# Kernel optimization log

Measured on AMD Instinct MI355X. Metric: run time of the kernel, lower is better.

The kernel has to match this reference:

```python
import jax, jax.numpy as jnp
import numpy as np

B, S, D = 4, 2048, 1024
H = 16
HD = D // H  # 64


def setup_inputs() -> dict:
    key = jax.random.key(0)
    ks = jax.random.split(key, 8)
    scale = 1.0 / np.sqrt(D)
    return {
        "hidden_states": jax.random.normal(ks[0], (B, S, D), dtype=jnp.float32),
        "attention_mask": jnp.ones((B, 1, 1, S), dtype=jnp.int32),
        "Wq": jax.random.normal(ks[1], (D, D), dtype=jnp.float32) * scale,
        "bq": jax.random.normal(ks[2], (D,), dtype=jnp.float32) * 0.02,
        "Wk": jax.random.normal(ks[3], (D, D), dtype=jnp.float32) * scale,
        "bk": jax.random.normal(ks[4], (D,), dtype=jnp.float32) * 0.02,
        "Wv": jax.random.normal(ks[5], (D, D), dtype=jnp.float32) * scale,
        "bv": jax.random.normal(ks[6], (D,), dtype=jnp.float32) * 0.02,
    }


def _split_heads(x):
    # [b, t, (h d)] -> [b, h, t, d]
    b, t, _ = x.shape
    return x.reshape(b, t, H, HD).transpose(0, 2, 1, 3)


def reference(hidden_states, attention_mask, Wq, bq, Wk, bk, Wv, bv):
    # Linear projections (torch Linear: x @ W.T + b)
    q = _split_heads(hidden_states @ Wq.T + bq)
    k = _split_heads(hidden_states @ Wk.T + bk)
    v = _split_heads(hidden_states @ Wv.T + bv)

    # scaled dot-product scores: [b, h, s, s]
    scores = jnp.einsum("bhqd,bhkd->bhqk", q, k) / np.sqrt(HD)

    s = scores.shape[-1]
    causal = jnp.tril(jnp.ones((s, s), dtype=bool))[None, None]
    neg_inf = jnp.float32(-jnp.inf)
    scores = jnp.where(causal, scores, neg_inf)
    # attention_mask is 0/1 keep mask: [b, 1, 1, s]
    scores = jnp.where(attention_mask == 0, neg_inf, scores)

    probs = jax.nn.softmax(scores, axis=-1)  # dropout p=0 (eval)
    ctx = jnp.einsum("bhqk,bhkd->bhqd", probs, v)
    # [b, h, t, d] -> [b, t, h*d]
    return ctx.transpose(0, 2, 1, 3).reshape(hidden_states.shape[0], s, D)
```

## Files before the change

kernel.cpp:

```cpp
#include <hip/hip_runtime.h>
#include <hip/hip_bf16.h>
#include <math.h>


#define B_ 4
#define S_ 2048
#define D_ 1024
#define H_ 16
#define HD_ 64
#define M_ (B_ * S_)

typedef unsigned short u16;
typedef unsigned int u32;
typedef __attribute__((ext_vector_type(4))) float f32x4;
typedef __attribute__((ext_vector_type(8))) short bf16x8;

__device__ __forceinline__ u16 f2bfu_rn(float x) {
    u32 u = __builtin_bit_cast(u32, x);
    return (u16)((u + 0x8000u) >> 16);
}

__device__ __forceinline__ void gl2lds16(const void* g, void* l) {
    __builtin_amdgcn_global_load_lds(
        (const __attribute__((address_space(1))) u32*)g,
        (__attribute__((address_space(3))) u32*)l, 16, 0, 0);
}

#define XN  8388608u
#define WN  1048576u
__global__ __launch_bounds__(256) void convert_bf16(
    const float* __restrict__ X,  const float* __restrict__ Wq,
    const float* __restrict__ Wk, const float* __restrict__ Wv,
    u16* __restrict__ Xb, u16* __restrict__ Wqb,
    u16* __restrict__ Wkb, u16* __restrict__ Wvb)
{
    size_t idx = ((size_t)blockIdx.x * 256 + threadIdx.x) * 8;
    const float* src; u16* dst; size_t off;
    if (idx < XN)                { src = X;  dst = Xb;  off = idx; }
    else if (idx < XN + WN)      { src = Wq; dst = Wqb; off = idx - XN; }
    else if (idx < XN + 2 * WN)  { src = Wk; dst = Wkb; off = idx - XN - WN; }
    else                         { src = Wv; dst = Wvb; off = idx - XN - 2 * WN; }
    float4 a = *(const float4*)(src + off);
    float4 b = *(const float4*)(src + off + 4);
    uint4 o;
    o.x = (u32)f2bfu_rn(a.x) | ((u32)f2bfu_rn(a.y) << 16);
    o.y = (u32)f2bfu_rn(a.z) | ((u32)f2bfu_rn(a.w) << 16);
    o.z = (u32)f2bfu_rn(b.x) | ((u32)f2bfu_rn(b.y) << 16);
    o.w = (u32)f2bfu_rn(b.z) | ((u32)f2bfu_rn(b.w) << 16);
    *(uint4*)(dst + off) = o;
}

#define QSCALE 0.18033688011112042f

__global__ __launch_bounds__(512) void qkv_mfma8(
    const u16* __restrict__ Xb,
    const u16* __restrict__ Wqb, const u16* __restrict__ Wkb,
    const u16* __restrict__ Wvb,
    const float* __restrict__ bq, const float* __restrict__ bk,
    const float* __restrict__ bv,
    u16* __restrict__ Qb, u16* __restrict__ Kb, u16* __restrict__ Vtb)
{
    const int which = blockIdx.y;
    const int bxl = ((blockIdx.x & 7) << 5) | (blockIdx.x >> 3);

    const u16* Asrc; const u16* Bsrc; const float* bias; u16* Out;
    int m0, n0;
    if (which == 0)      { Asrc = Xb;  Bsrc = Wqb; bias = bq; Out = Qb;
                           m0 = (bxl >> 2) * 128; n0 = (bxl & 3) * 256; }
    else if (which == 1) { Asrc = Xb;  Bsrc = Wkb; bias = bk; Out = Kb;
                           m0 = (bxl >> 2) * 128; n0 = (bxl & 3) * 256; }
    else                 { Asrc = Wvb; Bsrc = Xb;  bias = bv; Out = Vtb;
                           m0 = (bxl >> 5) * 128; n0 = (bxl & 31) * 256; }

    __shared__ u16 As[3][128][64];
    __shared__ u16 Bs[3][256][64];

    const int t = threadIdx.x;
    const int wave = t >> 6, lane = t & 63;
    const int qd = lane >> 4, l15 = lane & 15;
    const int wm = wave >> 2, wn = wave & 3;

    auto STAGE_A = [&](int tt, int u) {
        const int buf = tt % 3, k0 = tt * 64;
        const int rb = u * 64 + wave * 8;
        const int r  = rb + (lane >> 3);
        const int g  = (lane & 7) ^ (r & 7);
        gl2lds16(Asrc + (size_t)(m0 + r) * D_ + k0 + g * 8, &As[buf][rb][0]);
    };
    auto STAGE_B = [&](int tt, int q) {
        const int buf = tt % 3, k0 = tt * 64;
        const int rb = q * 64 + wave * 8;
        const int r  = rb + (lane >> 3);
        const int g  = (lane & 7) ^ (r & 7);
        gl2lds16(Bsrc + (size_t)(n0 + r) * D_ + k0 + g * 8, &Bs[buf][rb][0]);
    };

    const f32x4 zero = {0.f, 0.f, 0.f, 0.f};
    f32x4 acc[4][4];
#pragma unroll
    for (int i = 0; i < 4; ++i)
#pragma unroll
        for (int j = 0; j < 4; ++j) acc[i][j] = zero;

#pragma unroll
    for (int u = 0; u < 2; ++u) STAGE_A(0, u);
#pragma unroll
    for (int q = 0; q < 4; ++q) STAGE_B(0, q);
#pragma unroll
    for (int u = 0; u < 2; ++u) STAGE_A(1, u);
#pragma unroll
    for (int q = 0; q < 4; ++q) STAGE_B(1, q);
    asm volatile("s_waitcnt vmcnt(6)" ::: "memory");
    __builtin_amdgcn_s_barrier();

    for (int tt = 0; tt < 16; ++tt) {
        const int buf = tt % 3;
        const bool st = tt < 14;
        const int t2 = tt + 2;

        bf16x8 bfv[4][2];
        bf16x8 af[2];

#pragma unroll
        for (int nt = 0; nt < 4; ++nt) {
            const int row = wn * 64 + nt * 16 + l15;
#pragma unroll
            for (int ks = 0; ks < 2; ++ks)
                bfv[nt][ks] = *(const bf16x8*)&Bs[buf][row][((ks * 4 + qd) ^ (row & 7)) * 8];
        }
        {
            const int row = wm * 64 + l15;
#pragma unroll
            for (int ks = 0; ks < 2; ++ks)
                af[ks] = *(const bf16x8*)&As[buf][row][((ks * 4 + qd) ^ (row & 7)) * 8];
        }
        if (st) { STAGE_A(t2, 0); STAGE_A(t2, 1); }
        __builtin_amdgcn_s_barrier();
        asm volatile("s_waitcnt lgkmcnt(0)" ::: "memory");
        __builtin_amdgcn_sched_barrier(0);
        __builtin_amdgcn_s_setprio(1);
#pragma unroll
        for (int ks = 0; ks < 2; ++ks)
#pragma unroll
            for (int nt = 0; nt < 4; ++nt)
                acc[0][nt] = __builtin_amdgcn_mfma_f32_16x16x32_bf16(
                    af[ks], bfv[nt][ks], acc[0][nt], 0, 0, 0);
        __builtin_amdgcn_s_setprio(0);
        __builtin_amdgcn_s_barrier();

#pragma unroll
        for (int mt = 1; mt < 4; ++mt) {
            const int row = wm * 64 + mt * 16 + l15;
#pragma unroll
            for (int ks = 0; ks < 2; ++ks)
                af[ks] = *(const bf16x8*)&As[buf][row][((ks * 4 + qd) ^ (row & 7)) * 8];
            if (st) {
                if (mt == 1)      { STAGE_B(t2, 0); STAGE_B(t2, 1); }
                else if (mt == 2) { STAGE_B(t2, 2); }
                else              { STAGE_B(t2, 3); }
            }
            __builtin_amdgcn_s_barrier();
            asm volatile("s_waitcnt lgkmcnt(0)" ::: "memory");
            __builtin_amdgcn_sched_barrier(0);
            __builtin_amdgcn_s_setprio(1);
#pragma unroll
            for (int ks = 0; ks < 2; ++ks)
#pragma unroll
                for (int nt = 0; nt < 4; ++nt)
                    acc[mt][nt] = __builtin_amdgcn_mfma_f32_16x16x32_bf16(
                        af[ks], bfv[nt][ks], acc[mt][nt], 0, 0, 0);
            __builtin_amdgcn_s_setprio(0);
            if (mt == 3) {
                if (st) asm volatile("s_waitcnt vmcnt(6)" ::: "memory");
                else    asm volatile("s_waitcnt vmcnt(0)" ::: "memory");
            }
            __builtin_amdgcn_s_barrier();
        }
    }

    if (which < 2) {
#pragma unroll
        for (int nt = 0; nt < 4; ++nt) {
            int n = n0 + wn * 64 + nt * 16 + l15;
            float bv_ = bias[n];
            int h = n >> 6, hd = n & 63;
#pragma unroll
            for (int mt = 0; mt < 4; ++mt)
#pragma unroll
                for (int r = 0; r < 4; ++r) {
                    int m = m0 + wm * 64 + mt * 16 + qd * 4 + r;
                    int bb = m >> 11, s = m & 2047;
                    float v = acc[mt][nt][r] + bv_;
                    if (which == 0) v *= QSCALE;
                    Out[(((size_t)(bb * H_ + h)) * S_ + s) * HD_ + hd] = f2bfu_rn(v);
                }
        }
    } else {
#pragma unroll
        for (int mt = 0; mt < 4; ++mt)
#pragma unroll
            for (int r = 0; r < 4; ++r) {
                int f = m0 + wm * 64 + mt * 16 + qd * 4 + r;
                float bv_ = bias[f];
                int h = f >> 6, hd = f & 63;
#pragma unroll
                for (int nt = 0; nt < 4; ++nt) {
                    int tok = n0 + wn * 64 + nt * 16 + l15;
                    int bb = tok >> 11, s = tok & 2047;
                    float v = acc[mt][nt][r] + bv_;
                    Out[(((size_t)(bb * H_ + h)) * HD_ + hd) * S_ + s] = f2bfu_rn(v);
                }
            }
    }
}

__global__ __launch_bounds__(256) void attn_chunk(
    const u16* __restrict__ Qb, const u16* __restrict__ Kb,
    const u16* __restrict__ Vtb, const int* __restrict__ amask,
    float* __restrict__ Oout, float* __restrict__ Opart,
    float* __restrict__ L0, float* __restrict__ L1)
{
    const int bid = blockIdx.x;
    const int x   = bid >> 6;
    const int bh  = ((bid & 7) << 3) | ((bid >> 3) & 7);
    const int b = bh >> 4, h = bh & 15;
    int qt, jt0, jt1; bool second;
    if (x < 32) { qt = 31 - x; jt0 = 0;  jt1 = min(qt, 15); second = false; }
    else        { qt = 63 - x; jt0 = 16; jt1 = qt;          second = true;  }
    const int q0 = qt * 64;

    const int t = threadIdx.x;
    const int wave = t >> 6, lane = t & 63;
    const int qd = lane >> 4, l15 = lane & 15;

    __shared__ u16 Ks[64][64];
    __shared__ u16 Vts[64][64];
    __shared__ u16 Ps[64][72];
    __shared__ float mb[64];

    const size_t base = (size_t)bh * S_ * HD_;
    const u16* Qg = Qb + base;
    const u16* Kg = Kb + base;
    const u16* Vg = Vtb + base;
    const int* am = amask + b * S_;

    bf16x8 qf[2];
    {
        const u16* qrow = Qg + (size_t)(q0 + wave * 16 + l15) * HD_;
        qf[0] = *(const bf16x8*)(qrow + qd * 8);
        qf[1] = *(const bf16x8*)(qrow + 32 + qd * 8);
    }
    bf16x8 onesf;
    {
        short v = (l15 == 0) ? (short)0x3F80 : (short)0;
        onesf = (bf16x8){v, v, v, v, v, v, v, v};
    }

    const f32x4 zero = {0.f, 0.f, 0.f, 0.f};
    f32x4 o[5];
#pragma unroll
    for (int i = 0; i < 5; ++i) o[i] = zero;

    const int qloc = wave * 16 + l15;
    u32* prow32 = (u32*)&Ps[qloc][0];

    for (int jt = jt0; jt <= jt1; ++jt) {
        const int j0 = jt * 64;
        __syncthreads();
#pragma unroll
        for (int i = 0; i < 2; ++i) {
            int r0  = (wave * 2 + i) * 8;
            int row = r0 + (lane >> 3);
            int g   = (lane & 7) ^ (row & 7);
            gl2lds16(Kg + (size_t)(j0 + row) * HD_ + g * 8, &Ks[r0][0]);
            gl2lds16(Vg + (size_t)row * S_ + j0 + g * 8, &Vts[r0][0]);
        }
        if (t < 64) mb[t] = (am[j0 + t] == 0) ? -1e30f : 0.0f;
        __syncthreads();

        f32x4 sacc[4];
#pragma unroll
        for (int nt = 0; nt < 4; ++nt) sacc[nt] = zero;
        __builtin_amdgcn_s_setprio(1);
#pragma unroll
        for (int ks = 0; ks < 2; ++ks) {
#pragma unroll
            for (int nt = 0; nt < 4; ++nt) {
                int arow = nt * 16 + l15;
                int ap = (ks * 4 + qd) ^ (arow & 7);
                bf16x8 kf = *(const bf16x8*)&Ks[arow][ap * 8];
                sacc[nt] = __builtin_amdgcn_mfma_f32_16x16x32_bf16(
                    kf, qf[ks], sacc[nt], 0, 0, 0);
            }
        }
        __builtin_amdgcn_s_setprio(0);

        const bool diag = (jt == qt);
#pragma unroll
        for (int nt = 0; nt < 4; ++nt) {
            float4 m4 = *(const float4*)&mb[nt * 16 + qd * 4];
            float p[4];
#pragma unroll
            for (int r = 0; r < 4; ++r) {
                int kl = nt * 16 + qd * 4 + r;
                float s = sacc[nt][r] + ((const float*)&m4)[r];
                if (diag && kl > qloc) s = -1e30f;
                p[r] = __builtin_amdgcn_exp2f(s);
            }
            uint2 w;
            w.x = (u32)f2bfu_rn(p[0]) | ((u32)f2bfu_rn(p[1]) << 16);
            w.y = (u32)f2bfu_rn(p[2]) | ((u32)f2bfu_rn(p[3]) << 16);
            *(uint2*)&prow32[nt * 8 + qd * 2] = w;
        }

        __builtin_amdgcn_s_setprio(1);
#pragma unroll
        for (int ks = 0; ks < 2; ++ks) {
            int arow = wave * 16 + l15;
            bf16x8 pf = *(const bf16x8*)&Ps[arow][ks * 32 + qd * 8];
#pragma unroll
            for (int nt = 0; nt < 4; ++nt) {
                int brow = nt * 16 + l15;
                int bp = (ks * 4 + qd) ^ (brow & 7);
                bf16x8 vf = *(const bf16x8*)&Vts[brow][bp * 8];
                o[nt] = __builtin_amdgcn_mfma_f32_16x16x32_bf16(
                    pf, vf, o[nt], 0, 0, 0);
            }
            o[4] = __builtin_amdgcn_mfma_f32_16x16x32_bf16(
                pf, onesf, o[4], 0, 0, 0);
        }
        __builtin_amdgcn_s_setprio(0);
    }

    if (!second) {
        if (qt <= 15) {
#pragma unroll
            for (int r = 0; r < 4; ++r) {
                float l = __shfl(o[4][r], lane & 48);
                float inv = 1.0f / l;
                int q = q0 + wave * 16 + qd * 4 + r;
                float* op = Oout + ((size_t)(b * S_ + q)) * D_ + h * HD_;
#pragma unroll
                for (int nt = 0; nt < 4; ++nt)
                    op[nt * 16 + l15] = o[nt][r] * inv;
            }
        } else {
#pragma unroll
            for (int r = 0; r < 4; ++r) {
                int q = q0 + wave * 16 + qd * 4 + r;
                float* op = Oout + ((size_t)(b * S_ + q)) * D_ + h * HD_;
#pragma unroll
                for (int nt = 0; nt < 4; ++nt)
                    op[nt * 16 + l15] = o[nt][r];
                if (l15 == 0) L0[(size_t)bh * S_ + q] = o[4][r];
            }
        }
    } else {
#pragma unroll
        for (int r = 0; r < 4; ++r) {
            int q = q0 + wave * 16 + qd * 4 + r;
            int sh = q - 1024;
            float* op = Opart + ((size_t)bh * 1024 + sh) * HD_;
#pragma unroll
            for (int nt = 0; nt < 4; ++nt)
                op[nt * 16 + l15] = o[nt][r];
            if (l15 == 0) L1[(size_t)bh * 1024 + sh] = o[4][r];
        }
    }
}

__global__ __launch_bounds__(256) void combine(
    float* __restrict__ out, const float* __restrict__ Opart,
    const float* __restrict__ L0, const float* __restrict__ L1)
{
    size_t i = ((size_t)blockIdx.x * 256 + threadIdx.x) * 4;
    int d  = (int)(i & (D_ - 1));
    int bs = (int)(i >> 10);
    int b  = bs >> 10, sh = bs & 1023;
    int s  = sh + 1024;
    int h  = d >> 6;
    int bh = b * H_ + h;
    float l = L0[(size_t)bh * S_ + s] + L1[(size_t)bh * 1024 + sh];
    float inv = 1.0f / l;
    float* op = out + ((size_t)(b * S_ + s)) * D_ + d;
    const float* pp = Opart + ((size_t)bh * 1024 + sh) * HD_ + (d & 63);
    float4 v = *(float4*)op;
    float4 p = *(const float4*)pp;
    v.x = (v.x + p.x) * inv; v.y = (v.y + p.y) * inv;
    v.z = (v.z + p.z) * inv; v.w = (v.w + p.w) * inv;
    *(float4*)op = v;
}

extern "C" void kernel_launch(void* const* d_in, const int* in_sizes, int n_in,
                              void* d_out, int out_size, void* d_ws, size_t ws_size,
                              hipStream_t stream) {
    (void)in_sizes; (void)n_in; (void)out_size; (void)ws_size;
    const float* X    = (const float*)d_in[0];
    const int*   mask = (const int*)d_in[1];
    const float* Wq   = (const float*)d_in[2];
    const float* bq   = (const float*)d_in[3];
    const float* Wk   = (const float*)d_in[4];
    const float* bk   = (const float*)d_in[5];
    const float* Wv   = (const float*)d_in[6];
    const float* bv   = (const float*)d_in[7];
    float* out = (float*)d_out;

    u16* Xb  = (u16*)d_ws;
    u16* Wqb = Xb  + XN;
    u16* Wkb = Wqb + WN;
    u16* Wvb = Wkb + WN;
    u16* Qb  = Wvb + WN;
    u16* Kb  = Qb  + XN;
    u16* Vtb = Kb  + XN;
    float* Opart = (float*)(Vtb + XN);
    float* L0 = Opart + (size_t)64 * 1024 * 64;
    float* L1 = L0 + (size_t)64 * 2048;

    convert_bf16<<<(XN + 3 * WN) / (256 * 8), 256, 0, stream>>>(
        X, Wq, Wk, Wv, Xb, Wqb, Wkb, Wvb);
    qkv_mfma8<<<dim3(256, 3), 512, 0, stream>>>(
        Xb, Wqb, Wkb, Wvb, bq, bk, bv, Qb, Kb, Vtb);
    attn_chunk<<<dim3(3072), 256, 0, stream>>>(
        Qb, Kb, Vtb, mask, out, Opart, L0, L1);
    combine<<<(B_ * 1024 * D_ / 4) / 256, 256, 0, stream>>>(out, Opart, L0, L1);
}
```

Baseline: 243.8 us.

## Enlarge QKV GEMM tile to 256x256 with double-buffered LDS staging

```diff
diff --git a/kernel.cpp b/kernel.cpp
--- a/kernel.cpp
+++ b/kernel.cpp
@@ -61,19 +61,19 @@
     u16* __restrict__ Qb, u16* __restrict__ Kb, u16* __restrict__ Vtb)
 {
     const int which = blockIdx.y;
-    const int bxl = ((blockIdx.x & 7) << 5) | (blockIdx.x >> 3);
+    const int bxl = ((blockIdx.x & 7) << 4) | (blockIdx.x >> 3);
 
     const u16* Asrc; const u16* Bsrc; const float* bias; u16* Out;
     int m0, n0;
     if (which == 0)      { Asrc = Xb;  Bsrc = Wqb; bias = bq; Out = Qb;
-                           m0 = (bxl >> 2) * 128; n0 = (bxl & 3) * 256; }
+                           m0 = (bxl >> 2) * 256; n0 = (bxl & 3) * 256; }
     else if (which == 1) { Asrc = Xb;  Bsrc = Wkb; bias = bk; Out = Kb;
-                           m0 = (bxl >> 2) * 128; n0 = (bxl & 3) * 256; }
+                           m0 = (bxl >> 2) * 256; n0 = (bxl & 3) * 256; }
     else                 { Asrc = Wvb; Bsrc = Xb;  bias = bv; Out = Vtb;
-                           m0 = (bxl >> 5) * 128; n0 = (bxl & 31) * 256; }
-
-    __shared__ u16 As[3][128][64];
-    __shared__ u16 Bs[3][256][64];
+                           m0 = (bxl & 3) * 256; n0 = (bxl >> 2) * 256; }
+
+    __shared__ u16 As[2][256][64];
+    __shared__ u16 Bs[2][256][64];
 
     const int t = threadIdx.x;
     const int wave = t >> 6, lane = t & 63;
@@ -81,46 +81,47 @@
     const int wm = wave >> 2, wn = wave & 3;
 
     auto STAGE_A = [&](int tt, int u) {
-        const int buf = tt % 3, k0 = tt * 64;
+        const int buf = tt & 1, k0 = tt * 64;
         const int rb = u * 64 + wave * 8;
         const int r  = rb + (lane >> 3);
         const int g  = (lane & 7) ^ (r & 7);
         gl2lds16(Asrc + (size_t)(m0 + r) * D_ + k0 + g * 8, &As[buf][rb][0]);
     };
-    auto STAGE_B = [&](int tt, int q) {
-        const int buf = tt % 3, k0 = tt * 64;
-        const int rb = q * 64 + wave * 8;
+    auto STAGE_B = [&](int tt, int u) {
+        const int buf = tt & 1, k0 = tt * 64;
+        const int rb = u * 64 + wave * 8;
         const int r  = rb + (lane >> 3);
         const int g  = (lane & 7) ^ (r & 7);
         gl2lds16(Bsrc + (size_t)(n0 + r) * D_ + k0 + g * 8, &Bs[buf][rb][0]);
     };
 
     const f32x4 zero = {0.f, 0.f, 0.f, 0.f};
-    f32x4 acc[4][4];
-#pragma unroll
-    for (int i = 0; i < 4; ++i)
+    f32x4 acc[8][4];
+#pragma unroll
+    for (int i = 0; i < 8; ++i)
 #pragma unroll
         for (int j = 0; j < 4; ++j) acc[i][j] = zero;
 
 #pragma unroll
-    for (int u = 0; u < 2; ++u) STAGE_A(0, u);
-#pragma unroll
-    for (int q = 0; q < 4; ++q) STAGE_B(0, q);
-#pragma unroll
-    for (int u = 0; u < 2; ++u) STAGE_A(1, u);
-#pragma unroll
-    for (int q = 0; q < 4; ++q) STAGE_B(1, q);
-    asm volatile("s_waitcnt vmcnt(6)" ::: "memory");
+    for (int u = 0; u < 4; ++u) STAGE_A(0, u);
+#pragma unroll
+    for (int u = 0; u < 4; ++u) STAGE_B(0, u);
+    asm volatile("s_waitcnt vmcnt(0)" ::: "memory");
     __builtin_amdgcn_s_barrier();
 
     for (int tt = 0; tt < 16; ++tt) {
-        const int buf = tt % 3;
-        const bool st = tt < 14;
-        const int t2 = tt + 2;
+        const int buf = tt & 1;
+        const bool st = tt < 15;
 
         bf16x8 bfv[4][2];
-        bf16x8 af[2];
-
+        bf16x8 af[2][2];
+
+        if (st) {
+#pragma unroll
+            for (int u = 0; u < 4; ++u) STAGE_A(tt + 1, u);
+#pragma unroll
+            for (int u = 0; u < 4; ++u) STAGE_B(tt + 1, u);
+        }
 #pragma unroll
         for (int nt = 0; nt < 4; ++nt) {
             const int row = wn * 64 + nt * 16 + l15;
@@ -128,52 +129,52 @@
             for (int ks = 0; ks < 2; ++ks)
                 bfv[nt][ks] = *(const bf16x8*)&Bs[buf][row][((ks * 4 + qd) ^ (row & 7)) * 8];
         }
-        {
-            const int row = wm * 64 + l15;
+#pragma unroll
+        for (int i = 0; i < 2; ++i) {
+            const int row = wm * 128 + i * 16 + l15;
 #pragma unroll
             for (int ks = 0; ks < 2; ++ks)
-                af[ks] = *(const bf16x8*)&As[buf][row][((ks * 4 + qd) ^ (row & 7)) * 8];
-        }
-        if (st) { STAGE_A(t2, 0); STAGE_A(t2, 1); }
+                af[i][ks] = *(const bf16x8*)&As[buf][row][((ks * 4 + qd) ^ (row & 7)) * 8];
+        }
         __builtin_amdgcn_s_barrier();
         asm volatile("s_waitcnt lgkmcnt(0)" ::: "memory");
         __builtin_amdgcn_sched_barrier(0);
         __builtin_amdgcn_s_setprio(1);
 #pragma unroll
-        for (int ks = 0; ks < 2; ++ks)
-#pragma unroll
-            for (int nt = 0; nt < 4; ++nt)
-                acc[0][nt] = __builtin_amdgcn_mfma_f32_16x16x32_bf16(
-                    af[ks], bfv[nt][ks], acc[0][nt], 0, 0, 0);
+        for (int i = 0; i < 2; ++i)
+#pragma unroll
+            for (int ks = 0; ks < 2; ++ks)
+#pragma unroll
+                for (int nt = 0; nt < 4; ++nt)
+                    acc[i][nt] = __builtin_amdgcn_mfma_f32_16x16x32_bf16(
+                        af[i][ks], bfv[nt][ks], acc[i][nt], 0, 0, 0);
         __builtin_amdgcn_s_setprio(0);
         __builtin_amdgcn_s_barrier();
 
 #pragma unroll
-        for (int mt = 1; mt < 4; ++mt) {
-            const int row = wm * 64 + mt * 16 + l15;
-#pragma unroll
-            for (int ks = 0; ks < 2; ++ks)
-                af[ks] = *(const bf16x8*)&As[buf][row][((ks * 4 + qd) ^ (row & 7)) * 8];
-            if (st) {
-                if (mt == 1)      { STAGE_B(t2, 0); STAGE_B(t2, 1); }
-                else if (mt == 2) { STAGE_B(t2, 2); }
-                else              { STAGE_B(t2, 3); }
+        for (int pp = 1; pp < 4; ++pp) {
+#pragma unroll
+            for (int i = 0; i < 2; ++i) {
+                const int row = wm * 128 + (pp * 2 + i) * 16 + l15;
+#pragma unroll
+                for (int ks = 0; ks < 2; ++ks)
+                    af[i][ks] = *(const bf16x8*)&As[buf][row][((ks * 4 + qd) ^ (row & 7)) * 8];
             }
             __builtin_amdgcn_s_barrier();
             asm volatile("s_waitcnt lgkmcnt(0)" ::: "memory");
             __builtin_amdgcn_sched_barrier(0);
             __builtin_amdgcn_s_setprio(1);
 #pragma unroll
-            for (int ks = 0; ks < 2; ++ks)
-#pragma unroll
-                for (int nt = 0; nt < 4; ++nt)
-                    acc[mt][nt] = __builtin_amdgcn_mfma_f32_16x16x32_bf16(
-                        af[ks], bfv[nt][ks], acc[mt][nt], 0, 0, 0);
+            for (int i = 0; i < 2; ++i)
+#pragma unroll
+                for (int ks = 0; ks < 2; ++ks)
+#pragma unroll
+                    for (int nt = 0; nt < 4; ++nt)
+                        acc[pp * 2 + i][nt] = __builtin_amdgcn_mfma_f32_16x16x32_bf16(
+                            af[i][ks], bfv[nt][ks], acc[pp * 2 + i][nt], 0, 0, 0);
             __builtin_amdgcn_s_setprio(0);
-            if (mt == 3) {
-                if (st) asm volatile("s_waitcnt vmcnt(6)" ::: "memory");
-                else    asm volatile("s_waitcnt vmcnt(0)" ::: "memory");
-            }
+            if (pp == 3 && st)
+                asm volatile("s_waitcnt vmcnt(0)" ::: "memory");
             __builtin_amdgcn_s_barrier();
         }
     }
@@ -185,10 +186,10 @@
             float bv_ = bias[n];
             int h = n >> 6, hd = n & 63;
 #pragma unroll
-            for (int mt = 0; mt < 4; ++mt)
+            for (int mt = 0; mt < 8; ++mt)
 #pragma unroll
                 for (int r = 0; r < 4; ++r) {
-                    int m = m0 + wm * 64 + mt * 16 + qd * 4 + r;
+                    int m = m0 + wm * 128 + mt * 16 + qd * 4 + r;
                     int bb = m >> 11, s = m & 2047;
                     float v = acc[mt][nt][r] + bv_;
                     if (which == 0) v *= QSCALE;
@@ -197,10 +198,10 @@
         }
     } else {
 #pragma unroll
-        for (int mt = 0; mt < 4; ++mt)
+        for (int mt = 0; mt < 8; ++mt)
 #pragma unroll
             for (int r = 0; r < 4; ++r) {
-                int f = m0 + wm * 64 + mt * 16 + qd * 4 + r;
+                int f = m0 + wm * 128 + mt * 16 + qd * 4 + r;
                 float bv_ = bias[f];
                 int h = f >> 6, hd = f & 63;
 #pragma unroll
@@ -418,7 +419,7 @@
 
     convert_bf16<<<(XN + 3 * WN) / (256 * 8), 256, 0, stream>>>(
         X, Wq, Wk, Wv, Xb, Wqb, Wkb, Wvb);
-    qkv_mfma8<<<dim3(256, 3), 512, 0, stream>>>(
+    qkv_mfma8<<<dim3(128, 3), 512, 0, stream>>>(
         Xb, Wqb, Wkb, Wvb, bq, bk, bv, Qb, Kb, Vtb);
     attn_chunk<<<dim3(3072), 256, 0, stream>>>(
         Qb, Kb, Vtb, mask, out, Opart, L0, L1);
```

After: 251.8 us. 1.03x slower.
